# Optimization experiments

Hardware: AMD Instinct MI355X
Metric: run time of the kernel (lower is better)

Reference implementation:

```python
import jax, jax.numpy as jnp
import numpy as np

D_MODEL = 320
N_HEADS = 8
D_HEADS = 40
D_COND = 768
D_ATTN = N_HEADS * D_HEADS  # 320


def setup_inputs() -> dict:
    key = jax.random.key(0)
    ks = jax.random.split(key, 7)
    B, S, SK = 2, 4096, 4096
    x = jax.random.normal(ks[0], (B, S, D_MODEL), dtype=jnp.float32)
    cond = jax.random.normal(ks[1], (B, SK, D_COND), dtype=jnp.float32)
    # Linear weights stored as [in, out]; torch nn.Linear(in, out) has W [out, in],
    # applied as x @ W.T, equivalent to x @ W_here.
    sq = 1.0 / np.sqrt(D_MODEL)
    sc = 1.0 / np.sqrt(D_COND)
    sa = 1.0 / np.sqrt(D_ATTN)
    Wq = jax.random.uniform(ks[2], (D_MODEL, D_ATTN), jnp.float32, -sq, sq)
    Wk = jax.random.uniform(ks[3], (D_COND, D_ATTN), jnp.float32, -sc, sc)
    Wv = jax.random.uniform(ks[4], (D_COND, D_ATTN), jnp.float32, -sc, sc)
    Wo = jax.random.uniform(ks[5], (D_ATTN, D_MODEL), jnp.float32, -sa, sa)
    bo = jax.random.uniform(ks[6], (D_MODEL,), jnp.float32, -sa, sa)
    return {"x": x, "cond": cond, "Wq": Wq, "Wk": Wk, "Wv": Wv, "Wo": Wo, "bo": bo}


def reference(x, cond, Wq, Wk, Wv, Wo, bo):
    B, S, _ = x.shape
    SK = cond.shape[1]
    scale = D_HEADS ** -0.5
    q = (x @ Wq).reshape(B, S, N_HEADS, D_HEADS)      # [B,S,H,Dh]
    k = (cond @ Wk).reshape(B, SK, N_HEADS, D_HEADS)  # [B,SK,H,Dh]
    v = (cond @ Wv).reshape(B, SK, N_HEADS, D_HEADS)
    # materialized O(N^2) scores, as in the source (einsum -> softmax -> einsum)
    attn = jnp.einsum('bihd,bjhd->bhij', q, k) * scale  # [B,H,S,SK]
    attn = jax.nn.softmax(attn, axis=-1)
    out = jnp.einsum('bhij,bjhd->bihd', attn, v)        # [B,S,H,Dh]
    out = out.reshape(B, S, D_ATTN)
    return out @ Wo + bo
```

## Files before the change

### kernel.cpp

```cpp
#include <hip/hip_runtime.h>

typedef __attribute__((ext_vector_type(8))) short s16x8;
typedef __attribute__((ext_vector_type(4))) short s16x4;
typedef __attribute__((ext_vector_type(8))) __bf16 bf16x8;
typedef __attribute__((ext_vector_type(4))) float f32x4;
typedef __attribute__((ext_vector_type(4))) unsigned short u16x4;
typedef __attribute__((ext_vector_type(4))) unsigned int u32x4;

__device__ __forceinline__ f32x4 mfma_bf16(s16x8 a, s16x8 b, f32x4 c) {
  return __builtin_amdgcn_mfma_f32_16x16x32_bf16(
      __builtin_bit_cast(bf16x8, a), __builtin_bit_cast(bf16x8, b), c, 0, 0, 0);
}

__device__ __forceinline__ unsigned short f2bf(float f) {
  unsigned int u = __builtin_bit_cast(unsigned int, f);
  unsigned int r = u + 0x7FFFu + ((u >> 16) & 1u);
  return (unsigned short)(r >> 16);
}

__device__ __forceinline__ unsigned int cvt_pk_bf16(float lo, float hi) {
  unsigned int d;
  asm volatile("v_cvt_pk_bf16_f32 %0, %1, %2" : "=v"(d) : "v"(lo), "v"(hi));
  return d;
}

__global__ __launch_bounds__(256) void f32_to_bf16(const float* __restrict__ in,
                                                   unsigned short* __restrict__ out,
                                                   int n4) {
  int i = blockIdx.x * 256 + threadIdx.x;
  if (i < n4) {
    f32x4 v = ((const f32x4*)in)[i];
    u16x4 o;
    o[0] = f2bf(v[0]); o[1] = f2bf(v[1]); o[2] = f2bf(v[2]); o[3] = f2bf(v[3]);
    ((u16x4*)out)[i] = o;
  }
}

__global__ void transpose_f32_bf16(const float* __restrict__ in,
                                   unsigned short* __restrict__ out, int K, int N) {
  int id = blockIdx.x * 256 + threadIdx.x;
  if (id < K * N) {
    int k = id / N, n = id - k * N;
    out[(size_t)n * K + k] = f2bf(in[id]);
  }
}

template <int MODE>
__global__ __launch_bounds__(256) void gemm_direct(
    const unsigned short* __restrict__ A, const unsigned short* __restrict__ Wt,
    void* __restrict__ dstv, const float* __restrict__ bias, int K, float scale) {
  const int tid = threadIdx.x;
  const int l = tid & 63, w = tid >> 6;
  const int wm = w >> 1, wn = w & 1;
  const int lr = l & 15, lg = l >> 4;
  const int row0 = blockIdx.x * 64 + wm * 32;
  const int col0 = blockIdx.y * 64 + wn * 32;

  const unsigned short* Ap = A + (size_t)(row0 + lr) * K + lg * 8;
  const unsigned short* Bp = Wt + (size_t)(col0 + lr) * K + lg * 8;

  f32x4 acc[2][2];
#pragma unroll
  for (int i = 0; i < 2; i++)
#pragma unroll
    for (int j = 0; j < 2; j++) acc[i][j] = f32x4{0.f, 0.f, 0.f, 0.f};

  for (int k0 = 0; k0 < K; k0 += 32) {
    s16x8 a0 = *(const s16x8*)(Ap + k0);
    s16x8 a1 = *(const s16x8*)(Ap + (size_t)16 * K + k0);
    s16x8 b0 = *(const s16x8*)(Bp + k0);
    s16x8 b1 = *(const s16x8*)(Bp + (size_t)16 * K + k0);
    acc[0][0] = mfma_bf16(a0, b0, acc[0][0]);
    acc[0][1] = mfma_bf16(a0, b1, acc[0][1]);
    acc[1][0] = mfma_bf16(a1, b0, acc[1][0]);
    acc[1][1] = mfma_bf16(a1, b1, acc[1][1]);
  }

#pragma unroll
  for (int mf = 0; mf < 2; mf++)
#pragma unroll
    for (int nf = 0; nf < 2; nf++)
#pragma unroll
      for (int r = 0; r < 4; r++) {
        int m = row0 + mf * 16 + lg * 4 + r;
        int n = col0 + nf * 16 + lr;
        float v = acc[mf][nf][r];
        if (MODE == 0 || MODE == 1) {
          int b = m >> 12, s = m & 4095;
          int h = n / 40, d = n - h * 40;
          ((unsigned short*)dstv)[((size_t)(b * 8 + h) * 4096 + s) * 64 + d] =
              f2bf(v * scale);
        } else if (MODE == 2) {
          int b = m >> 12, s = m & 4095;
          int h = n / 40, d = n - h * 40;
          ((unsigned short*)dstv)[((size_t)(b * 8 + h) * 48 + d) * 4096 + s] = f2bf(v);
        } else {
          ((float*)dstv)[(size_t)m * 320 + n] = v + bias[n];
        }
      }
}

__global__ __launch_bounds__(512) void attn_kernel(
    const unsigned short* __restrict__ Qh, const unsigned short* __restrict__ Kh,
    const unsigned short* __restrict__ Vt, unsigned short* __restrict__ AO) {
  __shared__ __align__(16) char kt[8192];
  __shared__ __align__(16) char vts[6144];

  const int tid = threadIdx.x;
  const int l = tid & 63, w = tid >> 6;
  const int lr = l & 15, lg = l >> 4;
  const int bh = blockIdx.y;
  const int b = bh >> 3, h = bh & 7;
  const int qbase = blockIdx.x * 128;
  const int qrow = qbase + w * 16 + lr;

  const unsigned short* Qp = Qh + ((size_t)bh * 4096 + qbase + w * 16) * 64;
  const unsigned short* Kp = Kh + (size_t)bh * 4096 * 64;
  const unsigned short* Vp = Vt + (size_t)bh * 48 * 4096;

  s16x8 q0 = *(const s16x8*)(Qp + lr * 64 + lg * 8);
  s16x8 q1 = *(const s16x8*)(Qp + lr * 64 + 32 + lg * 8);

  f32x4 O[3];
#pragma unroll
  for (int nf = 0; nf < 3; nf++) O[nf] = f32x4{0.f, 0.f, 0.f, 0.f};
  float rm = -1e30f, rl = 0.f;

  for (int kb = 0; kb < 4096; kb += 64) {
    __syncthreads();
    {
      int row = tid >> 3, ch = tid & 7;
      s16x8 tv = *(const s16x8*)(Kp + (size_t)(kb + row) * 64 + ch * 8);
      *(s16x8*)(kt + ((row * 128 + ch * 16) ^ ((row & 7) << 4))) = tv;
    }
    if (tid < 384) {
      int row = tid >> 3, ch = tid & 7;
      s16x8 tv = *(const s16x8*)(Vp + (size_t)row * 4096 + kb + ch * 8);
      *(s16x8*)(vts + ((row * 128 + ch * 16) ^ ((row & 7) << 4))) = tv;
    }
    __syncthreads();

    f32x4 sf[4];
#pragma unroll
    for (int nf = 0; nf < 4; nf++) sf[nf] = f32x4{0.f, 0.f, 0.f, 0.f};
#pragma unroll
    for (int nf = 0; nf < 4; nf++) {
      int krow = nf * 16 + lr;
      s16x8 kf0 = *(const s16x8*)(kt + ((krow * 128 + lg * 16) ^ ((krow & 7) << 4)));
      s16x8 kf1 = *(const s16x8*)(kt + ((krow * 128 + 64 + lg * 16) ^ ((krow & 7) << 4)));
      sf[nf] = mfma_bf16(kf0, q0, sf[nf]);
      sf[nf] = mfma_bf16(kf1, q1, sf[nf]);
    }

    float tm = fmaxf(fmaxf(fmaxf(sf[0][0], sf[0][1]), fmaxf(sf[0][2], sf[0][3])),
                     fmaxf(fmaxf(sf[1][0], sf[1][1]), fmaxf(sf[1][2], sf[1][3])));
    tm = fmaxf(tm, fmaxf(fmaxf(fmaxf(sf[2][0], sf[2][1]), fmaxf(sf[2][2], sf[2][3])),
                         fmaxf(fmaxf(sf[3][0], sf[3][1]), fmaxf(sf[3][2], sf[3][3]))));
    tm = fmaxf(tm, __shfl_xor(tm, 16, 64));
    tm = fmaxf(tm, __shfl_xor(tm, 32, 64));
    float mn = fmaxf(rm, tm);
    float al = __builtin_amdgcn_exp2f(rm - mn);
    rm = mn;
    rl *= al;
#pragma unroll
    for (int nf = 0; nf < 3; nf++) {
#pragma unroll
      for (int r = 0; r < 4; r++) O[nf][r] *= al;
    }
    float ts = 0.f;
    unsigned int pk[4][2];
#pragma unroll
    for (int nf = 0; nf < 4; nf++) {
      float p0 = __builtin_amdgcn_exp2f(sf[nf][0] - rm);
      float p1 = __builtin_amdgcn_exp2f(sf[nf][1] - rm);
      float p2 = __builtin_amdgcn_exp2f(sf[nf][2] - rm);
      float p3 = __builtin_amdgcn_exp2f(sf[nf][3] - rm);
      ts += (p0 + p1) + (p2 + p3);
      pk[nf][0] = cvt_pk_bf16(p0, p1);
      pk[nf][1] = cvt_pk_bf16(p2, p3);
    }
    ts += __shfl_xor(ts, 16, 64);
    ts += __shfl_xor(ts, 32, 64);
    rl += ts;

#pragma unroll
    for (int c = 0; c < 2; c++) {
      u32x4 bu = {pk[2 * c][0], pk[2 * c][1], pk[2 * c + 1][0], pk[2 * c + 1][1]};
      s16x8 bfrag = __builtin_bit_cast(s16x8, bu);
#pragma unroll
      for (int nf = 0; nf < 3; nf++) {
        int row = nf * 16 + lr;
        int base = row * 128 + c * 64 + lg * 8;
        int swz = (row & 7) << 4;
        s16x4 a0 = *(const s16x4*)(vts + ((base) ^ swz));
        s16x4 a1 = *(const s16x4*)(vts + ((base + 32) ^ swz));
        s16x8 afrag = {a0[0], a0[1], a0[2], a0[3], a1[0], a1[1], a1[2], a1[3]};
        O[nf] = mfma_bf16(afrag, bfrag, O[nf]);
      }
    }
  }

  float inv = 1.f / rl;
#pragma unroll
  for (int nf = 0; nf < 3; nf++) {
#pragma unroll
    for (int r = 0; r < 4; r++) {
      int d = nf * 16 + lg * 4 + r;
      if (d < 40) {
        AO[((size_t)(b * 4096 + qrow)) * 320 + h * 40 + d] = f2bf(O[nf][r] * inv);
      }
    }
  }
}

extern "C" void kernel_launch(void* const* d_in, const int* in_sizes, int n_in,
                              void* d_out, int out_size, void* d_ws,
                              size_t ws_size, hipStream_t stream) {
  const float* x    = (const float*)d_in[0];
  const float* cond = (const float*)d_in[1];
  const float* Wq   = (const float*)d_in[2];
  const float* Wk   = (const float*)d_in[3];
  const float* Wv   = (const float*)d_in[4];
  const float* Wo   = (const float*)d_in[5];
  const float* bo   = (const float*)d_in[6];

  char* ws = (char*)d_ws;
  unsigned short* xb    = (unsigned short*)(ws + 0);
  unsigned short* condb = (unsigned short*)(ws + 5242880);
  unsigned short* WtQ   = (unsigned short*)(ws + 17825792);
  unsigned short* WtK   = (unsigned short*)(ws + 18030592);
  unsigned short* WtV   = (unsigned short*)(ws + 18522112);
  unsigned short* WtO   = (unsigned short*)(ws + 19013632);
  unsigned short* AO    = (unsigned short*)(ws + 19218432);
  unsigned short* Qh    = (unsigned short*)(ws + 24461312);
  unsigned short* Kh    = (unsigned short*)(ws + 32849920);
  unsigned short* Vt    = (unsigned short*)(ws + 41238528);

  hipMemsetAsync(Qh, 0, 23068672, stream);

  f32_to_bf16<<<dim3(2560), 256, 0, stream>>>(x, xb, 655360);
  f32_to_bf16<<<dim3(6144), 256, 0, stream>>>(cond, condb, 1572864);

  transpose_f32_bf16<<<dim3(400), 256, 0, stream>>>(Wq, WtQ, 320, 320);
  transpose_f32_bf16<<<dim3(960), 256, 0, stream>>>(Wk, WtK, 768, 320);
  transpose_f32_bf16<<<dim3(960), 256, 0, stream>>>(Wv, WtV, 768, 320);
  transpose_f32_bf16<<<dim3(400), 256, 0, stream>>>(Wo, WtO, 320, 320);

  const float qscale = 1.44269504088896f / sqrtf(40.0f);

  gemm_direct<0><<<dim3(128, 5), 256, 0, stream>>>(xb, WtQ, Qh, nullptr, 320, qscale);
  gemm_direct<1><<<dim3(128, 5), 256, 0, stream>>>(condb, WtK, Kh, nullptr, 768, 1.0f);
  gemm_direct<2><<<dim3(128, 5), 256, 0, stream>>>(condb, WtV, Vt, nullptr, 768, 1.0f);

  attn_kernel<<<dim3(32, 16), 512, 0, stream>>>(Qh, Kh, Vt, AO);

  gemm_direct<3><<<dim3(128, 5), 256, 0, stream>>>(AO, WtO, d_out, bo, 320, 1.0f);
}
```

Measured before the change: 309.4 us.

## Prefetch K/V tiles into registers and double-buffer GEMM loads

The attention kernel now loads the next K and V tiles into registers during the current tile's compute and writes them to shared memory at the end of the iteration, so global loads overlap the MFMA and softmax work. It also skips the running-max rescale when no lane's max grew, and raises wave priority around the MFMA blocks. The projection GEMMs take K as a template parameter and are fully unrolled with register double-buffered operand loads. This adds register pressure and keeps two barriers per iteration.

```diff
diff --git a/kernel.cpp b/kernel.cpp
--- a/kernel.cpp
+++ b/kernel.cpp
@@ -45,10 +45,10 @@
   }
 }
 
-template <int MODE>
+template <int MODE, int K>
 __global__ __launch_bounds__(256) void gemm_direct(
     const unsigned short* __restrict__ A, const unsigned short* __restrict__ Wt,
-    void* __restrict__ dstv, const float* __restrict__ bias, int K, float scale) {
+    void* __restrict__ dstv, const float* __restrict__ bias, float scale) {
   const int tid = threadIdx.x;
   const int l = tid & 63, w = tid >> 6;
   const int wm = w >> 1, wn = w & 1;
@@ -65,15 +65,27 @@
 #pragma unroll
     for (int j = 0; j < 2; j++) acc[i][j] = f32x4{0.f, 0.f, 0.f, 0.f};
 
-  for (int k0 = 0; k0 < K; k0 += 32) {
-    s16x8 a0 = *(const s16x8*)(Ap + k0);
-    s16x8 a1 = *(const s16x8*)(Ap + (size_t)16 * K + k0);
-    s16x8 b0 = *(const s16x8*)(Bp + k0);
-    s16x8 b1 = *(const s16x8*)(Bp + (size_t)16 * K + k0);
-    acc[0][0] = mfma_bf16(a0, b0, acc[0][0]);
-    acc[0][1] = mfma_bf16(a0, b1, acc[0][1]);
-    acc[1][0] = mfma_bf16(a1, b0, acc[1][0]);
-    acc[1][1] = mfma_bf16(a1, b1, acc[1][1]);
+  constexpr int NB = K / 32;
+  s16x8 a0[2], a1[2], b0[2], b1[2];
+  a0[0] = *(const s16x8*)(Ap);
+  a1[0] = *(const s16x8*)(Ap + (size_t)16 * K);
+  b0[0] = *(const s16x8*)(Bp);
+  b1[0] = *(const s16x8*)(Bp + (size_t)16 * K);
+
+#pragma unroll
+  for (int i = 0; i < NB; i++) {
+    const int cur = i & 1, nxt = cur ^ 1;
+    if (i + 1 < NB) {
+      const int k = (i + 1) * 32;
+      a0[nxt] = *(const s16x8*)(Ap + k);
+      a1[nxt] = *(const s16x8*)(Ap + (size_t)16 * K + k);
+      b0[nxt] = *(const s16x8*)(Bp + k);
+      b1[nxt] = *(const s16x8*)(Bp + (size_t)16 * K + k);
+    }
+    acc[0][0] = mfma_bf16(a0[cur], b0[cur], acc[0][0]);
+    acc[0][1] = mfma_bf16(a0[cur], b1[cur], acc[0][1]);
+    acc[1][0] = mfma_bf16(a1[cur], b0[cur], acc[1][0]);
+    acc[1][1] = mfma_bf16(a1[cur], b1[cur], acc[1][1]);
   }
 
 #pragma unroll
@@ -118,6 +130,10 @@
   const unsigned short* Kp = Kh + (size_t)bh * 4096 * 64;
   const unsigned short* Vp = Vt + (size_t)bh * 48 * 4096;
 
+  const int srow = tid >> 3, sch = tid & 7;
+  const bool hasv = (tid < 384);
+  const int kofs = ((srow * 128 + sch * 16) ^ ((srow & 7) << 4));
+
   s16x8 q0 = *(const s16x8*)(Qp + lr * 64 + lg * 8);
   s16x8 q1 = *(const s16x8*)(Qp + lr * 64 + 32 + lg * 8);
 
@@ -126,23 +142,23 @@
   for (int nf = 0; nf < 3; nf++) O[nf] = f32x4{0.f, 0.f, 0.f, 0.f};
   float rm = -1e30f, rl = 0.f;
 
+  s16x8 kreg = *(const s16x8*)(Kp + (size_t)srow * 64 + sch * 8);
+  s16x8 vreg;
+  if (hasv) vreg = *(const s16x8*)(Vp + (size_t)srow * 4096 + sch * 8);
+  *(s16x8*)(kt + kofs) = kreg;
+  if (hasv) *(s16x8*)(vts + kofs) = vreg;
+  __syncthreads();
+
   for (int kb = 0; kb < 4096; kb += 64) {
-    __syncthreads();
-    {
-      int row = tid >> 3, ch = tid & 7;
-      s16x8 tv = *(const s16x8*)(Kp + (size_t)(kb + row) * 64 + ch * 8);
-      *(s16x8*)(kt + ((row * 128 + ch * 16) ^ ((row & 7) << 4))) = tv;
-    }
-    if (tid < 384) {
-      int row = tid >> 3, ch = tid & 7;
-      s16x8 tv = *(const s16x8*)(Vp + (size_t)row * 4096 + kb + ch * 8);
-      *(s16x8*)(vts + ((row * 128 + ch * 16) ^ ((row & 7) << 4))) = tv;
-    }
-    __syncthreads();
+    if (kb + 64 < 4096) {
+      kreg = *(const s16x8*)(Kp + (size_t)(kb + 64 + srow) * 64 + sch * 8);
+      if (hasv) vreg = *(const s16x8*)(Vp + (size_t)srow * 4096 + kb + 64 + sch * 8);
+    }
 
     f32x4 sf[4];
 #pragma unroll
     for (int nf = 0; nf < 4; nf++) sf[nf] = f32x4{0.f, 0.f, 0.f, 0.f};
+    __builtin_amdgcn_s_setprio(1);
 #pragma unroll
     for (int nf = 0; nf < 4; nf++) {
       int krow = nf * 16 + lr;
@@ -151,6 +167,7 @@
       sf[nf] = mfma_bf16(kf0, q0, sf[nf]);
       sf[nf] = mfma_bf16(kf1, q1, sf[nf]);
     }
+    __builtin_amdgcn_s_setprio(0);
 
     float tm = fmaxf(fmaxf(fmaxf(sf[0][0], sf[0][1]), fmaxf(sf[0][2], sf[0][3])),
                      fmaxf(fmaxf(sf[1][0], sf[1][1]), fmaxf(sf[1][2], sf[1][3])));
@@ -158,14 +175,16 @@
                          fmaxf(fmaxf(sf[3][0], sf[3][1]), fmaxf(sf[3][2], sf[3][3]))));
     tm = fmaxf(tm, __shfl_xor(tm, 16, 64));
     tm = fmaxf(tm, __shfl_xor(tm, 32, 64));
-    float mn = fmaxf(rm, tm);
-    float al = __builtin_amdgcn_exp2f(rm - mn);
-    rm = mn;
-    rl *= al;
-#pragma unroll
-    for (int nf = 0; nf < 3; nf++) {
-#pragma unroll
-      for (int r = 0; r < 4; r++) O[nf][r] *= al;
+    if (!__all(tm <= rm)) {
+      float mn = fmaxf(rm, tm);
+      float al = __builtin_amdgcn_exp2f(rm - mn);
+      rm = mn;
+      rl *= al;
+#pragma unroll
+      for (int nf = 0; nf < 3; nf++) {
+#pragma unroll
+        for (int r = 0; r < 4; r++) O[nf][r] *= al;
+      }
     }
     float ts = 0.f;
     unsigned int pk[4][2];
@@ -183,6 +202,7 @@
     ts += __shfl_xor(ts, 32, 64);
     rl += ts;
 
+    __builtin_amdgcn_s_setprio(1);
 #pragma unroll
     for (int c = 0; c < 2; c++) {
       u32x4 bu = {pk[2 * c][0], pk[2 * c][1], pk[2 * c + 1][0], pk[2 * c + 1][1]};
@@ -198,6 +218,14 @@
         O[nf] = mfma_bf16(afrag, bfrag, O[nf]);
       }
     }
+    __builtin_amdgcn_s_setprio(0);
+
+    __syncthreads();
+    if (kb + 64 < 4096) {
+      *(s16x8*)(kt + kofs) = kreg;
+      if (hasv) *(s16x8*)(vts + kofs) = vreg;
+    }
+    __syncthreads();
   }
 
   float inv = 1.f / rl;
@@ -248,11 +276,11 @@
 
   const float qscale = 1.44269504088896f / sqrtf(40.0f);
 
-  gemm_direct<0><<<dim3(128, 5), 256, 0, stream>>>(xb, WtQ, Qh, nullptr, 320, qscale);
-  gemm_direct<1><<<dim3(128, 5), 256, 0, stream>>>(condb, WtK, Kh, nullptr, 768, 1.0f);
-  gemm_direct<2><<<dim3(128, 5), 256, 0, stream>>>(condb, WtV, Vt, nullptr, 768, 1.0f);
+  gemm_direct<0, 320><<<dim3(128, 5), 256, 0, stream>>>(xb, WtQ, Qh, nullptr, qscale);
+  gemm_direct<1, 768><<<dim3(128, 5), 256, 0, stream>>>(condb, WtK, Kh, nullptr, 1.0f);
+  gemm_direct<2, 768><<<dim3(128, 5), 256, 0, stream>>>(condb, WtV, Vt, nullptr, 1.0f);
 
   attn_kernel<<<dim3(32, 16), 512, 0, stream>>>(Qh, Kh, Vt, AO);
 
-  gemm_direct<3><<<dim3(128, 5), 256, 0, stream>>>(AO, WtO, d_out, bo, 320, 1.0f);
-}
+  gemm_direct<3, 320><<<dim3(128, 5), 256, 0, stream>>>(AO, WtO, d_out, bo, 1.0f);
+}
```

Result: faster. 294.9 us (-4.7%).
